# Performance work log

Hardware: AMD Instinct MI355X
Metric: run time of the kernel (lower is better)

The kernel has to match this reference:

```python
import jax, jax.numpy as jnp
import numpy as np

N_NODES = 1024
CHANNELS = [1, 64, 128]
DENSE = [196608, 256]
SAMPLE_NUMBER = 50


def _glorot(key, shape):
    fan_in, fan_out = shape[0], shape[-1]
    s = jnp.sqrt(6.0 / (fan_in + fan_out))
    return jax.random.uniform(key, shape, jnp.float32, -s, s)


def setup_inputs() -> dict:
    key = jax.random.key(0)
    ks = jax.random.split(key, 20)
    T, B = 16, 64
    inp = {
        "xs_seq": jax.random.normal(ks[0], (T, B, N_NODES, CHANNELS[0]), jnp.float32),
        "adj": jax.random.uniform(ks[1], (N_NODES, N_NODES), jnp.float32) / N_NODES,
    }
    # GCGRU params per layer: gates z, r, candidate n over concat([x, h])
    ki = 2
    for li in range(len(CHANNELS) - 1):
        cin, cout = CHANNELS[li], CHANNELS[li + 1]
        for g in ("z", "r", "n"):
            inp[f"W{g}{li}"] = _glorot(ks[ki], (cin + cout, cout)); ki += 1
            inp[f"b{g}{li}"] = jnp.zeros((cout,), jnp.float32)
    inp["W_mu"] = _glorot(ks[ki], (DENSE[0], DENSE[1])); ki += 1
    inp["b_mu"] = jnp.zeros((DENSE[1],), jnp.float32)
    inp["W_lv"] = _glorot(ks[ki], (DENSE[0], DENSE[1])); ki += 1
    inp["b_lv"] = jnp.zeros((DENSE[1],), jnp.float32)
    return inp


def _gcgru(xs, adj, Wz, bz, Wr, br, Wn, bn, cout):
    # xs: [T, B, N, cin]; graph-conv GRU over time via scan
    T, B, N, _ = xs.shape
    h0 = jnp.zeros((B, N, cout), xs.dtype)

    def gconv(a, x, W, b):  # adj @ x @ W + b
        return jnp.einsum("ij,bjc,cd->bid", a, x, W) + b

    def step(h, x):
        xh = jnp.concatenate([x, h], axis=-1)
        z = jax.nn.sigmoid(gconv(adj, xh, Wz, bz))
        r = jax.nn.sigmoid(gconv(adj, xh, Wr, br))
        xrh = jnp.concatenate([x, r * h], axis=-1)
        n = jnp.tanh(gconv(adj, xrh, Wn, bn))
        h_new = (1.0 - z) * h + z * n
        return h_new, h_new

    _, hs = jax.lax.scan(step, h0, xs)
    return hs  # [T, B, N, cout]


def _forward(xs_seq, adj, Wz0, bz0, Wr0, br0, Wn0, bn0,
             Wz1, bz1, Wr1, br1, Wn1, bn1, W_mu, b_mu, W_lv, b_lv, eps):
    h1 = _gcgru(xs_seq, adj, Wz0, bz0, Wr0, br0, Wn0, bn0, CHANNELS[1])
    h2 = _gcgru(h1, adj, Wz1, bz1, Wr1, br1, Wn1, bn1, CHANNELS[2])
    xs = jnp.concatenate([h1[-1], h2[-1]], axis=2)  # [B, N, C1+C2]
    B = xs.shape[0]
    xs = xs.reshape(B, -1)  # [B, N*(C1+C2)]
    mu = jax.nn.sigmoid(xs @ W_mu + b_mu)
    logvar = jax.nn.sigmoid(xs @ W_lv + b_lv)
    std = jnp.exp(0.5 * logvar)
    z = mu + eps * std
    return z, mu, logvar


def reference(xs_seq, adj, Wz0, bz0, Wr0, br0, Wn0, bn0,
              Wz1, bz1, Wr1, br1, Wn1, bn1, W_mu, b_mu, W_lv, b_lv):
    B = xs_seq.shape[1]
    ekey = jax.random.fold_in(jax.random.key(0), 1234)
    eps = jax.random.normal(ekey, (SAMPLE_NUMBER, B, DENSE[1]), jnp.float32).mean(0)
    return _forward(xs_seq, adj, Wz0, bz0, Wr0, br0, Wn0, bn0,
                    Wz1, bz1, Wr1, br1, Wn1, bn1, W_mu, b_mu, W_lv, b_lv, eps)
```

## Files before the change

kernel.cpp:

```cpp
#include <hip/hip_runtime.h>
#include <math.h>

#define EPS_MODE 0

typedef unsigned short u16;
typedef short bf16x8 __attribute__((ext_vector_type(8)));
typedef float f32x4 __attribute__((ext_vector_type(4)));
typedef u16 u16x4 __attribute__((ext_vector_type(4)));
typedef u16 u16x8 __attribute__((ext_vector_type(8)));

static constexpr int T = 16;
static constexpr size_t MF = 1u << 20;
static constexpr int DKCH = 512;
static constexpr int DKCHUNK = 196608 / DKCH;

__device__ __forceinline__ u16 f2bf(float f) {
  unsigned u = __float_as_uint(f);
  unsigned r = (u + 0x7fffu + ((u >> 16) & 1u)) >> 16;
  return (u16)r;
}
__device__ __forceinline__ float bf2f(u16 h) {
  return __uint_as_float(((unsigned)h) << 16);
}
__device__ __forceinline__ void gload16(const void* g, void* l) {
  __builtin_amdgcn_global_load_lds(
      (const __attribute__((address_space(1))) void*)g,
      (__attribute__((address_space(3))) void*)l, 16, 0, 0);
}
__device__ __forceinline__ float sigm(float x) { return 1.f / (1.f + expf(-x)); }

__global__ __launch_bounds__(256) void cast_bf16(const float* __restrict__ in,
                                                 u16* __restrict__ out, int n) {
  int i = (blockIdx.x * 256 + threadIdx.x) * 4;
  if (i < n) {
    float4 v = *reinterpret_cast<const float4*>(&in[i]);
    out[i + 0] = f2bf(v.x); out[i + 1] = f2bf(v.y);
    out[i + 2] = f2bf(v.z); out[i + 3] = f2bf(v.w);
  }
}

__global__ __launch_bounds__(256) void prep_wt(const float* __restrict__ Wz0, const float* __restrict__ Wr0,
                                               const float* __restrict__ Wn0, const float* __restrict__ Wz1,
                                               const float* __restrict__ Wr1, const float* __restrict__ Wn1,
                                               u16* __restrict__ WzrT0, u16* __restrict__ WnT0,
                                               u16* __restrict__ WzrT1, u16* __restrict__ WnT1) {
  int seg = blockIdx.y;
  int idx = blockIdx.x * 256 + threadIdx.x;
  if (seg == 0) {
    if (idx < 128 * 64) {
      int j = idx >> 6, k = idx & 63;
      float v = (j < 64) ? Wz0[(k + 1) * 64 + j] : Wr0[(k + 1) * 64 + (j - 64)];
      WzrT0[idx] = f2bf(v);
    }
  } else if (seg == 1) {
    if (idx < 64 * 64) {
      int j = idx >> 6, k = idx & 63;
      WnT0[idx] = f2bf(Wn0[(k + 1) * 64 + j]);
    }
  } else if (seg == 2) {
    if (idx < 256 * 192) {
      int j = idx / 192, k = idx % 192;
      float v = (j < 128) ? Wz1[k * 128 + j] : Wr1[k * 128 + (j - 128)];
      WzrT1[idx] = f2bf(v);
    }
  } else {
    if (idx < 128 * 192) {
      int j = idx / 192, k = idx % 192;
      WnT1[idx] = f2bf(Wn1[k * 128 + j]);
    }
  }
}

__global__ __launch_bounds__(256) void init0(const float* __restrict__ AXv,
                                             const float* __restrict__ Wz0,
                                             const float* __restrict__ bz0,
                                             const float* __restrict__ Wn0,
                                             const float* __restrict__ bn0,
                                             u16* __restrict__ h1T) {
  int b = blockIdx.x, n0 = blockIdx.y * 256;
  __shared__ float axs[256];
  int tid = threadIdx.x;
  if (tid < 64)
    *(float4*)&axs[tid * 4] = *(const float4*)&AXv[((size_t)b << 10) + n0 + tid * 4];
  __syncthreads();
  int cb = tid >> 6, nl = (tid & 63) * 4;
  for (int c0 = 0; c0 < 64; c0 += 4) {
    int c = c0 + cb;
    float wz = Wz0[c], bz = bz0[c], wn = Wn0[c], bn = bn0[c];
    u16x4 pk;
#pragma unroll
    for (int j = 0; j < 4; ++j) {
      float ax = axs[nl + j];
      float z = sigm(fmaf(ax, wz, bz));
      pk[j] = f2bf(z * tanhf(fmaf(ax, wn, bn)));
    }
    *(u16x4*)&h1T[((((size_t)b << 6) + c) << 10) + n0 + nl] = pk;
  }
}

template <int EPI, int LOGC, int MFR>
__device__ __forceinline__ void dev_adj_mfma(int bx, int by, char* lds,
                                             const u16* __restrict__ A,
                                             const u16* __restrict__ BT,
                                             void* __restrict__ OUT) {
  constexpr int MT = MFR * 32;
  int tid = threadIdx.x;
  int w = tid >> 6, lane = tid & 63;
  int row0 = by * MT, col0 = bx * 128;
  int wm = w >> 1, wn = w & 1;
  f32x4 acc[MFR][4] = {};
  for (int k0 = 0; k0 < 1024; k0 += 64) {
#pragma unroll
    for (int q = 0; q < MFR; ++q) {
      int row = q * 32 + w * 8 + (lane >> 3);
      gload16(A + (size_t)(row0 + row) * 1024 + k0 + (lane & 7) * 8,
              lds + q * 4096 + w * 1024);
    }
#pragma unroll
    for (int q = 0; q < 4; ++q) {
      int row = q * 32 + w * 8 + (lane >> 3);
      gload16(BT + (size_t)(col0 + row) * 1024 + k0 + (lane & 7) * 8,
              lds + MFR * 4096 + q * 4096 + w * 1024);
    }
    __syncthreads();
#pragma unroll
    for (int kk = 0; kk < 2; ++kk) {
      bf16x8 a[MFR], bb[4];
#pragma unroll
      for (int m = 0; m < MFR; ++m)
        a[m] = *(const bf16x8*)(lds + (wm * (MFR * 16) + m * 16 + (lane & 15)) * 128 + kk * 64 + (lane >> 4) * 16);
#pragma unroll
      for (int n = 0; n < 4; ++n)
        bb[n] = *(const bf16x8*)(lds + MFR * 4096 + (wn * 64 + n * 16 + (lane & 15)) * 128 + kk * 64 + (lane >> 4) * 16);
#pragma unroll
      for (int m = 0; m < MFR; ++m)
#pragma unroll
        for (int n = 0; n < 4; ++n)
          acc[m][n] = __builtin_amdgcn_mfma_f32_16x16x32_bf16(a[m], bb[n], acc[m][n], 0, 0, 0);
    }
    __syncthreads();
  }
  if (EPI == 1) {
    float* O = (float*)OUT;
#pragma unroll
    for (int m = 0; m < MFR; ++m)
#pragma unroll
      for (int n = 0; n < 4; ++n) {
        int col = col0 + wn * 64 + n * 16 + (lane & 15);
        int t = col >> 6, bbx = col & 63;
        int row = row0 + wm * (MFR * 16) + m * 16 + ((lane >> 4) << 2);
        *(float4*)&O[((size_t)t << 16) + ((size_t)bbx << 10) + row] = *(float4*)&acc[m][n];
      }
  } else {
    u16* O = (u16*)OUT;
    constexpr int C = 1 << LOGC;
#pragma unroll
    for (int m = 0; m < MFR; ++m)
#pragma unroll
      for (int n = 0; n < 4; ++n) {
        int col = col0 + wn * 64 + n * 16 + (lane & 15);
        int bbx = col >> LOGC, c = col & (C - 1);
#pragma unroll
        for (int j = 0; j < 4; ++j) {
          int row = row0 + wm * (MFR * 16) + m * 16 + ((lane >> 4) << 2) + j;
          O[(((size_t)bbx << 10) + row) * C + c] = f2bf(acc[m][n][j]);
        }
      }
  }
}

template <int EPI, int LOGC, int MFR>
__global__ __launch_bounds__(256) void adj_mfma(const u16* __restrict__ A,
                                                const u16* __restrict__ BT,
                                                void* __restrict__ OUT) {
  __shared__ __align__(16) char lds[(MFR + 4) * 4096];
  dev_adj_mfma<EPI, LOGC, MFR>(blockIdx.x, blockIdx.y, lds, A, BT, OUT);
}

template <int C, int RK1, int MFR>
__device__ __forceinline__ void dev_adj_ngate(
    int bx, int by, char* lds,
    const u16* __restrict__ A, const u16* __restrict__ BT,
    const u16* __restrict__ WnT, const float* __restrict__ bias,
    const float* __restrict__ axv, const float* __restrict__ wx,
    const u16* __restrict__ AH1, const u16* __restrict__ zT,
    u16* __restrict__ hT) {
  constexpr int LOGC = (C == 64) ? 6 : 7;
  constexpr int KW = (C == 64) ? 64 : 192;
  constexpr int KKAN = C / 32;
  constexpr int MT = MFR * 32;
  int tid = threadIdx.x;
  int w = tid >> 6, lane = tid & 63;
  int row0 = by * MT, col0 = bx * 128;
  int wm = w >> 1, wn = w & 1;
  f32x4 acc[MFR][4] = {};
  for (int k0 = 0; k0 < 1024; k0 += 64) {
#pragma unroll
    for (int q = 0; q < MFR; ++q) {
      int row = q * 32 + w * 8 + (lane >> 3);
      gload16(A + (size_t)(row0 + row) * 1024 + k0 + (lane & 7) * 8,
              lds + q * 4096 + w * 1024);
    }
#pragma unroll
    for (int q = 0; q < 4; ++q) {
      int row = q * 32 + w * 8 + (lane >> 3);
      gload16(BT + (size_t)(col0 + row) * 1024 + k0 + (lane & 7) * 8,
              lds + MFR * 4096 + q * 4096 + w * 1024);
    }
    __syncthreads();
#pragma unroll
    for (int kk = 0; kk < 2; ++kk) {
      bf16x8 a[MFR], bb[4];
#pragma unroll
      for (int m = 0; m < MFR; ++m)
        a[m] = *(const bf16x8*)(lds + (wm * (MFR * 16) + m * 16 + (lane & 15)) * 128 + kk * 64 + (lane >> 4) * 16);
#pragma unroll
      for (int n = 0; n < 4; ++n)
        bb[n] = *(const bf16x8*)(lds + MFR * 4096 + (wn * 64 + n * 16 + (lane & 15)) * 128 + kk * 64 + (lane >> 4) * 16);
#pragma unroll
      for (int m = 0; m < MFR; ++m)
#pragma unroll
        for (int n = 0; n < 4; ++n)
          acc[m][n] = __builtin_amdgcn_mfma_f32_16x16x32_bf16(a[m], bb[n], acc[m][n], 0, 0, 0);
    }
    __syncthreads();
  }
  u16* ANt = (u16*)lds;
#pragma unroll
  for (int m = 0; m < MFR; ++m)
#pragma unroll
    for (int n = 0; n < 4; ++n) {
      int cl = wn * 64 + n * 16 + (lane & 15);
      int rl = wm * (MFR * 16) + m * 16 + ((lane >> 4) << 2);
#pragma unroll
      for (int j = 0; j < 4; ++j)
        ANt[(rl + j) * 136 + cl] = f2bf(acc[m][n][j]);
    }
  __syncthreads();
  int wrow = w >> 1, half = w & 1;
  int arow0 = wrow * (MFR * 16);
  int b0 = col0 >> LOGC;
  int out0 = (C == 64) ? 0 : half * 64;
  int kbase = (C == 64) ? half * 64 : 0;
  int b_eff = (C == 64) ? (b0 + half) : b0;
  constexpr int WOFF = (C == 64) ? 0 : 64;
  f32x4 acc2[MFR][4] = {};
#pragma unroll
  for (int kk = 0; kk < KKAN; ++kk) {
    bf16x8 a[MFR], bb[4];
    int ka = kbase + kk * 32 + (lane >> 4) * 8;
#pragma unroll
    for (int m = 0; m < MFR; ++m)
      a[m] = *(const bf16x8*)&ANt[(arow0 + m * 16 + (lane & 15)) * 136 + ka];
#pragma unroll
    for (int n = 0; n < 4; ++n)
      bb[n] = *(const bf16x8*)&WnT[(size_t)(out0 + n * 16 + (lane & 15)) * KW + WOFF + kk * 32 + (lane >> 4) * 8];
#pragma unroll
    for (int m = 0; m < MFR; ++m)
#pragma unroll
      for (int n = 0; n < 4; ++n)
        acc2[m][n] = __builtin_amdgcn_mfma_f32_16x16x32_bf16(a[m], bb[n], acc2[m][n], 0, 0, 0);
  }
  if (C == 128) {
#pragma unroll
    for (int kk = 0; kk < 2; ++kk) {
      bf16x8 a[MFR], bb[4];
#pragma unroll
      for (int m = 0; m < MFR; ++m)
        a[m] = *(const bf16x8*)&AH1[(((size_t)b0 << 10) + row0 + arow0 + m * 16 + (lane & 15)) * 64 + kk * 32 + (lane >> 4) * 8];
#pragma unroll
      for (int n = 0; n < 4; ++n)
        bb[n] = *(const bf16x8*)&WnT[(size_t)(out0 + n * 16 + (lane & 15)) * 192 + kk * 32 + (lane >> 4) * 8];
#pragma unroll
      for (int m = 0; m < MFR; ++m)
#pragma unroll
        for (int n = 0; n < 4; ++n)
          acc2[m][n] = __builtin_amdgcn_mfma_f32_16x16x32_bf16(a[m], bb[n], acc2[m][n], 0, 0, 0);
    }
  }
#pragma unroll
  for (int m = 0; m < MFR; ++m) {
    float ax4[4];
    if (RK1) {
      float4 v = *(const float4*)&axv[((size_t)b_eff << 10) + row0 + arow0 + m * 16 + ((lane >> 4) << 2)];
      ax4[0] = v.x; ax4[1] = v.y; ax4[2] = v.z; ax4[3] = v.w;
    }
#pragma unroll
    for (int n = 0; n < 4; ++n) {
      int cp = out0 + n * 16 + (lane & 15);
      int grow = arow0 + m * 16 + ((lane >> 4) << 2);
      size_t idx = (((size_t)b_eff << LOGC) + cp) * 1024 + row0 + grow;
      u16x4 zv = *(const u16x4*)&zT[idx];
      u16x4 hv = *(const u16x4*)&hT[idx];
      u16x4 pk;
#pragma unroll
      for (int j = 0; j < 4; ++j) {
        float g = acc2[m][n][j] + bias[cp];
        if (RK1) g += ax4[j] * wx[cp];
        float nv = tanhf(g);
        float z = bf2f(zv[j]), ho = bf2f(hv[j]);
        pk[j] = f2bf((1.f - z) * ho + z * nv);
      }
      *(u16x4*)&hT[idx] = pk;
    }
  }
}

template <int C, int RK1, int MFR>
__global__ __launch_bounds__(256) void adj_ngate(
    const u16* __restrict__ A, const u16* __restrict__ BT,
    const u16* __restrict__ WnT, const float* __restrict__ bias,
    const float* __restrict__ axv, const float* __restrict__ wx,
    const u16* __restrict__ AH1, const u16* __restrict__ zT,
    u16* __restrict__ hT) {
  constexpr int MT = MFR * 32;
  constexpr int STG = (MFR + 4) * 4096;
  constexpr int ANB = MT * 136 * 2;
  constexpr int LDSZ = STG > ANB ? STG : ANB;
  __shared__ __align__(16) char lds[LDSZ];
  dev_adj_ngate<C, RK1, MFR>(blockIdx.x, blockIdx.y, lds, A, BT, WnT, bias, axv, wx,
                             AH1, zT, hT);
}

__global__ __launch_bounds__(256) void combo_tail(
    const u16* __restrict__ adjB, const u16* __restrict__ h2T, u16* __restrict__ AH2,
    const u16* __restrict__ rh0T, const u16* __restrict__ WnT0, const float* __restrict__ bn0,
    const float* __restrict__ AXt1, const float* __restrict__ Wn0,
    const u16* __restrict__ z0T, u16* __restrict__ h1T) {
  __shared__ __align__(16) char lds[32768];
  int bid = blockIdx.x;
  if (bid < 512) {
    dev_adj_mfma<0, 7, 4>(bid & 63, bid >> 6, lds, adjB, h2T, AH2);
  } else {
    int b2 = bid - 512;
    dev_adj_ngate<64, 1, 2>(b2 & 31, b2 >> 5, lds, adjB, rh0T, WnT0, bn0,
                            AXt1, Wn0, nullptr, z0T, h1T);
  }
}

__global__ __launch_bounds__(256) void ah1_zr(
    const u16* __restrict__ adjB, const u16* __restrict__ h1T,
    const u16* __restrict__ AH2, const u16* __restrict__ h2T,
    const u16* __restrict__ WzrT1, const float* __restrict__ bz1, const float* __restrict__ br1,
    const u16* __restrict__ WzrT0, const float* __restrict__ bz0, const float* __restrict__ br0,
    const float* __restrict__ AXt1, const float* __restrict__ wz0x, const float* __restrict__ wr0x,
    u16* __restrict__ AH1, u16* __restrict__ z1T, u16* __restrict__ rh1T,
    u16* __restrict__ z0T, u16* __restrict__ rh0T, int do_zr0) {
  __shared__ __align__(16) char lds[24576];
  int tid = threadIdx.x, w = tid >> 6, lane = tid & 63;
  int row0 = blockIdx.y * 64, col0 = blockIdx.x * 128;
  int b0 = col0 >> 6;
  int wm = w >> 1, wn = w & 1;
  f32x4 acc[2][4] = {};
  for (int k0 = 0; k0 < 1024; k0 += 64) {
#pragma unroll
    for (int q = 0; q < 2; ++q) {
      int row = q * 32 + w * 8 + (lane >> 3);
      gload16(adjB + (size_t)(row0 + row) * 1024 + k0 + (lane & 7) * 8,
              lds + q * 4096 + w * 1024);
    }
#pragma unroll
    for (int q = 0; q < 4; ++q) {
      int row = q * 32 + w * 8 + (lane >> 3);
      gload16(h1T + (size_t)(col0 + row) * 1024 + k0 + (lane & 7) * 8,
              lds + 8192 + q * 4096 + w * 1024);
    }
    __syncthreads();
#pragma unroll
    for (int kk = 0; kk < 2; ++kk) {
      bf16x8 a[2], bb[4];
#pragma unroll
      for (int m = 0; m < 2; ++m)
        a[m] = *(const bf16x8*)(lds + (wm * 32 + m * 16 + (lane & 15)) * 128 + kk * 64 + (lane >> 4) * 16);
#pragma unroll
      for (int n = 0; n < 4; ++n)
        bb[n] = *(const bf16x8*)(lds + 8192 + (wn * 64 + n * 16 + (lane & 15)) * 128 + kk * 64 + (lane >> 4) * 16);
#pragma unroll
      for (int m = 0; m < 2; ++m)
#pragma unroll
        for (int n = 0; n < 4; ++n)
          acc[m][n] = __builtin_amdgcn_mfma_f32_16x16x32_bf16(a[m], bb[n], acc[m][n], 0, 0, 0);
    }
    __syncthreads();
  }
  u16* ANt = (u16*)lds;
#pragma unroll
  for (int m = 0; m < 2; ++m)
#pragma unroll
    for (int n = 0; n < 4; ++n) {
      int col = wn * 64 + n * 16 + (lane & 15);
      int bl = col >> 6, c = col & 63;
      int rl = wm * 32 + m * 16 + ((lane >> 4) << 2);
#pragma unroll
      for (int j = 0; j < 4; ++j) {
        u16 v = f2bf(acc[m][n][j]);
        AH1[(((size_t)(b0 + bl) << 10) + row0 + rl + j) * 64 + c] = v;
        ANt[(bl * 64 + rl + j) * 72 + c] = v;
      }
    }
  __syncthreads();
  int b = b0 + wm;
#pragma unroll
  for (int hz = 0; hz < 2; ++hz) {
    f32x4 g1[4][4] = {};
#pragma unroll
    for (int kk = 0; kk < 2; ++kk) {
      bf16x8 a[4], bb[4];
#pragma unroll
      for (int m = 0; m < 4; ++m)
        a[m] = *(const bf16x8*)&ANt[(wm * 64 + m * 16 + (lane & 15)) * 72 + kk * 32 + (lane >> 4) * 8];
#pragma unroll
      for (int n = 0; n < 4; ++n) {
        int out = hz * 128 + wn * 64 + n * 16 + (lane & 15);
        bb[n] = *(const bf16x8*)&WzrT1[(size_t)out * 192 + kk * 32 + (lane >> 4) * 8];
      }
#pragma unroll
      for (int m = 0; m < 4; ++m)
#pragma unroll
        for (int n = 0; n < 4; ++n)
          g1[m][n] = __builtin_amdgcn_mfma_f32_16x16x32_bf16(a[m], bb[n], g1[m][n], 0, 0, 0);
    }
#pragma unroll
    for (int kk = 0; kk < 4; ++kk) {
      bf16x8 a[4], bb[4];
#pragma unroll
      for (int m = 0; m < 4; ++m) {
        int gn = row0 + m * 16 + (lane & 15);
        a[m] = *(const bf16x8*)&AH2[(((size_t)b << 10) + gn) * 128 + kk * 32 + (lane >> 4) * 8];
      }
#pragma unroll
      for (int n = 0; n < 4; ++n) {
        int out = hz * 128 + wn * 64 + n * 16 + (lane & 15);
        bb[n] = *(const bf16x8*)&WzrT1[(size_t)out * 192 + 64 + kk * 32 + (lane >> 4) * 8];
      }
#pragma unroll
      for (int m = 0; m < 4; ++m)
#pragma unroll
        for (int n = 0; n < 4; ++n)
          g1[m][n] = __builtin_amdgcn_mfma_f32_16x16x32_bf16(a[m], bb[n], g1[m][n], 0, 0, 0);
    }
#pragma unroll
    for (int m = 0; m < 4; ++m)
#pragma unroll
      for (int n = 0; n < 4; ++n) {
        int outq = hz * 128 + wn * 64 + n * 16 + (lane & 15);
        bool iz = outq < 128;
        int c = iz ? outq : outq - 128;
        int gr = m * 16 + ((lane >> 4) << 2);
        size_t idx = (((size_t)b * 128 + c) << 10) + row0 + gr;
        u16x4 hv;
        if (!iz) hv = *(const u16x4*)&h2T[idx];
        u16x4 pk;
#pragma unroll
        for (int j = 0; j < 4; ++j) {
          float g = g1[m][n][j] + (iz ? bz1 : br1)[c];
          float sg = sigm(g);
          pk[j] = iz ? f2bf(sg) : f2bf(sg * bf2f(hv[j]));
        }
        *(u16x4*)&(iz ? z1T : rh1T)[idx] = pk;
      }
  }
  if (do_zr0) {
    f32x4 g0[4][4] = {};
#pragma unroll
    for (int kk = 0; kk < 2; ++kk) {
      bf16x8 a[4], bb[4];
#pragma unroll
      for (int m = 0; m < 4; ++m)
        a[m] = *(const bf16x8*)&ANt[(wm * 64 + m * 16 + (lane & 15)) * 72 + kk * 32 + (lane >> 4) * 8];
#pragma unroll
      for (int n = 0; n < 4; ++n) {
        int out = wn * 64 + n * 16 + (lane & 15);
        bb[n] = *(const bf16x8*)&WzrT0[(size_t)out * 64 + kk * 32 + (lane >> 4) * 8];
      }
#pragma unroll
      for (int m = 0; m < 4; ++m)
#pragma unroll
        for (int n = 0; n < 4; ++n)
          g0[m][n] = __builtin_amdgcn_mfma_f32_16x16x32_bf16(a[m], bb[n], g0[m][n], 0, 0, 0);
    }
#pragma unroll
    for (int m = 0; m < 4; ++m) {
      int gr0 = m * 16 + ((lane >> 4) << 2);
      float4 av = *(const float4*)&AXt1[((size_t)b << 10) + row0 + gr0];
      float ax4[4] = {av.x, av.y, av.z, av.w};
#pragma unroll
      for (int n = 0; n < 4; ++n) {
        int out = wn * 64 + n * 16 + (lane & 15);
        bool iz = out < 64;
        int c = out & 63;
        size_t idx = (((size_t)b * 64 + c) << 10) + row0 + gr0;
        u16x4 hv;
        if (!iz) hv = *(const u16x4*)&h1T[idx];
        u16x4 pk;
#pragma unroll
        for (int j = 0; j < 4; ++j) {
          float g = g0[m][n][j] + (iz ? bz0 : br0)[c] + ax4[j] * (iz ? wz0x : wr0x)[c];
          float sg = sigm(g);
          pk[j] = iz ? f2bf(sg) : f2bf(sg * bf2f(hv[j]));
        }
        *(u16x4*)&(iz ? z0T : rh0T)[idx] = pk;
      }
    }
  }
}

__global__ __launch_bounds__(256) void transpose_x(const u16* __restrict__ h1T,
                                                   const u16* __restrict__ h2T,
                                                   u16* __restrict__ X) {
  int b = blockIdx.x;
  int n0 = blockIdx.y * 128;
  __shared__ u16 tile[192][136];
  int tid = threadIdx.x;
#pragma unroll
  for (int i = 0; i < 12; ++i) {
    int id = tid + i * 256;
    int c = id >> 4, g = id & 15;
    u16x8 v;
    if (c < 64) v = *(const u16x8*)&h1T[(((size_t)b << 6) + c) * 1024 + n0 + g * 8];
    else        v = *(const u16x8*)&h2T[(((size_t)b << 7) + (c - 64)) * 1024 + n0 + g * 8];
    *(u16x8*)&tile[c][g * 8] = v;
  }
  __syncthreads();
#pragma unroll
  for (int i = 0; i < 12; ++i) {
    int id = tid + i * 256;
    int n = id / 24, g = id % 24;
    u16x8 v;
#pragma unroll
    for (int j = 0; j < 8; ++j) v[j] = tile[g * 8 + j][n];
    *(u16x8*)&X[(size_t)b * 196608 + (size_t)(n0 + n) * 192 + g * 8] = v;
  }
}

__global__ __launch_bounds__(256) void dense_mfma4(const u16* __restrict__ X,
                                                   const float* __restrict__ Wmu,
                                                   const float* __restrict__ Wlv,
                                                   float* __restrict__ P) {
  __shared__ __align__(16) char lds[8192 + 128 * 70 * 2];
  u16* Bs = (u16*)(lds + 8192);
  int tid = threadIdx.x, w = tid >> 6, lane = tid & 63;
  int o0 = blockIdx.x * 128;
  int ch = blockIdx.y, mat = blockIdx.z;
  const float* W = mat ? Wlv : Wmu;
  int kb = ch * DKCHUNK;
  int oq = (tid & 31) * 4;
  int kq = (tid >> 5) * 8;
  f32x4 acc[4][2] = {};
  float4 wv[8];
  {
    const float* wp = W + (size_t)(kb + kq) * 256 + o0 + oq;
#pragma unroll
    for (int p = 0; p < 8; ++p) wv[p] = *(const float4*)(wp + (size_t)p * 256);
  }
  for (int s = 0; s < DKCHUNK / 64; ++s) {
    int kg = kb + s * 64;
#pragma unroll
    for (int q = 0; q < 2; ++q) {
      int row = q * 32 + w * 8 + (lane >> 3);
      gload16(X + (size_t)row * 196608 + kg + (lane & 7) * 8,
              lds + q * 4096 + w * 1024);
    }
#pragma unroll
    for (int j = 0; j < 4; ++j) {
      u16x8 pk;
#pragma unroll
      for (int p = 0; p < 8; ++p) pk[p] = f2bf(wv[p][j]);
      *(u16x8*)&Bs[(oq + j) * 70 + kq] = pk;
    }
    __syncthreads();
    if (s + 1 < DKCHUNK / 64) {
      const float* wp = W + (size_t)(kg + 64 + kq) * 256 + o0 + oq;
#pragma unroll
      for (int p = 0; p < 8; ++p) wv[p] = *(const float4*)(wp + (size_t)p * 256);
    }
#pragma unroll
    for (int kk = 0; kk < 2; ++kk) {
      bf16x8 a[4], bb[2];
#pragma unroll
      for (int m = 0; m < 4; ++m)
        a[m] = *(const bf16x8*)(lds + (m * 16 + (lane & 15)) * 128 + kk * 64 + (lane >> 4) * 16);
#pragma unroll
      for (int n = 0; n < 2; ++n) {
        int o = w * 32 + n * 16 + (lane & 15);
        bb[n] = *(const bf16x8*)&Bs[o * 70 + kk * 32 + (lane >> 4) * 8];
      }
#pragma unroll
      for (int m = 0; m < 4; ++m)
#pragma unroll
        for (int n = 0; n < 2; ++n)
          acc[m][n] = __builtin_amdgcn_mfma_f32_16x16x32_bf16(a[m], bb[n], acc[m][n], 0, 0, 0);
    }
    __syncthreads();
  }
#pragma unroll
  for (int m = 0; m < 4; ++m)
#pragma unroll
    for (int n = 0; n < 2; ++n) {
      int o = o0 + w * 32 + n * 16 + (lane & 15);
#pragma unroll
      for (int j = 0; j < 4; ++j) {
        int row = m * 16 + ((lane >> 4) << 2) + j;
        P[(((size_t)mat * DKCH + ch) * 64 + row) * 256 + o] = acc[m][n][j];
      }
    }
}

__device__ __forceinline__ unsigned rotl32(unsigned v, int s) {
  return (v << s) | (v >> (32 - s));
}
__device__ void threefry(unsigned k0, unsigned k1, unsigned x0, unsigned x1,
                         unsigned& o0, unsigned& o1) {
  unsigned ks2 = k0 ^ k1 ^ 0x1BD11BDAu;
  unsigned a = x0 + k0, b = x1 + k1;
#define TF_RND(rot) { a += b; b = rotl32(b, rot); b ^= a; }
  TF_RND(13) TF_RND(15) TF_RND(26) TF_RND(6)
  a += k1; b += ks2 + 1u;
  TF_RND(17) TF_RND(29) TF_RND(16) TF_RND(24)
  a += ks2; b += k0 + 2u;
  TF_RND(13) TF_RND(15) TF_RND(26) TF_RND(6)
  a += k0; b += k1 + 3u;
  TF_RND(17) TF_RND(29) TF_RND(16) TF_RND(24)
  a += k1; b += ks2 + 4u;
  TF_RND(13) TF_RND(15) TF_RND(26) TF_RND(6)
  a += ks2; b += k0 + 5u;
#undef TF_RND
  o0 = a; o1 = b;
}

__device__ float u32_to_normal(unsigned bits) {
  unsigned fb = (bits >> 9) | 0x3F800000u;
  float f = __uint_as_float(fb) - 1.0f;
  const float lo = -0.99999994f;
  float u = f * 2.0f + lo;
  u = fmaxf(lo, u);
  float w = -log1pf(-u * u);
  float p;
  if (w < 5.0f) {
    w -= 2.5f;
    p = 2.81022636e-08f;
    p = fmaf(p, w, 3.43273939e-07f);
    p = fmaf(p, w, -3.5233877e-06f);
    p = fmaf(p, w, -4.39150654e-06f);
    p = fmaf(p, w, 0.00021858087f);
    p = fmaf(p, w, -0.00125372503f);
    p = fmaf(p, w, -0.00417768164f);
    p = fmaf(p, w, 0.246640727f);
    p = fmaf(p, w, 1.50140941f);
  } else {
    w = sqrtf(w) - 3.0f;
    p = -0.000200214257f;
    p = fmaf(p, w, 0.000100950558f);
    p = fmaf(p, w, 0.00134934322f);
    p = fmaf(p, w, -0.00367342844f);
    p = fmaf(p, w, 0.00573950773f);
    p = fmaf(p, w, -0.0076224613f);
    p = fmaf(p, w, 0.00943887047f);
    p = fmaf(p, w, 1.00167406f);
    p = fmaf(p, w, 2.83297682f);
  }
  return 1.41421354f * (p * u);
}

__global__ __launch_bounds__(256) void eps_kernel(float* __restrict__ eps) {
  int b = blockIdx.x;
  int o = threadIdx.x;
  unsigned k0, k1;
  threefry(0u, 0u, 0u, 1234u, k0, k1);
  float s = 0.f;
  for (int smp = 0; smp < 50; ++smp) {
    unsigned idx = ((unsigned)smp * 64u + (unsigned)b) * 256u + (unsigned)o;
    unsigned o0, o1, bits;
#if EPS_MODE == 0
    threefry(k0, k1, 0u, idx, o0, o1);
    bits = o0 ^ o1;
#else
    unsigned pp = idx % 409600u, half = idx / 409600u;
    threefry(k0, k1, pp, pp + 409600u, o0, o1);
    bits = half ? o1 : o0;
#endif
    s += u32_to_normal(bits);
  }
  eps[b * 256 + o] = s / 50.0f;
}

__global__ __launch_bounds__(256) void final_kernel(const float* __restrict__ P,
                                                    const float* __restrict__ bmu,
                                                    const float* __restrict__ blv,
                                                    const float* __restrict__ eps,
                                                    float* __restrict__ out) {
  int b = blockIdx.x, o = threadIdx.x;
  float smu = 0.f, slv = 0.f;
  for (int ch = 0; ch < DKCH; ++ch) {
    smu += P[(((size_t)0 * DKCH + ch) * 64 + b) * 256 + o];
    slv += P[(((size_t)1 * DKCH + ch) * 64 + b) * 256 + o];
  }
  float mu = sigm(smu + bmu[o]);
  float lv = sigm(slv + blv[o]);
  float z = mu + eps[b * 256 + o] * expf(0.5f * lv);
  out[b * 256 + o] = z;
  out[16384 + b * 256 + o] = mu;
  out[32768 + b * 256 + o] = lv;
}

extern "C" void kernel_launch(void* const* d_in, const int* in_sizes, int n_in,
                              void* d_out, int out_size, void* d_ws, size_t ws_size,
                              hipStream_t stream) {
  (void)in_sizes; (void)n_in; (void)out_size; (void)ws_size;
  const float* xs  = (const float*)d_in[0];
  const float* adj = (const float*)d_in[1];
  const float* Wz0 = (const float*)d_in[2];  const float* bz0 = (const float*)d_in[3];
  const float* Wr0 = (const float*)d_in[4];  const float* br0 = (const float*)d_in[5];
  const float* Wn0 = (const float*)d_in[6];  const float* bn0 = (const float*)d_in[7];
  const float* Wz1 = (const float*)d_in[8];  const float* bz1 = (const float*)d_in[9];
  const float* Wr1 = (const float*)d_in[10]; const float* br1 = (const float*)d_in[11];
  const float* Wn1 = (const float*)d_in[12]; const float* bn1 = (const float*)d_in[13];
  const float* Wmu = (const float*)d_in[14]; const float* bmu = (const float*)d_in[15];
  const float* Wlv = (const float*)d_in[16]; const float* blv = (const float*)d_in[17];

  float* ws = (float*)d_ws;
  u16*  adjB  = (u16*)(ws);
  u16*  xsB   = (u16*)(ws + MF / 2);
  float* AXv  = ws + 1 * MF;
  u16*  h1T   = (u16*)(ws + 2 * MF);
  u16*  h2T   = (u16*)(ws + 4 * MF);
  u16*  z0T   = (u16*)(ws + 8 * MF);
  u16*  z1T   = (u16*)(ws + 10 * MF);
  u16*  rh0T  = (u16*)(ws + 14 * MF);
  u16*  rh1T  = (u16*)(ws + 16 * MF);
  u16*  AH1   = (u16*)(ws + 20 * MF);
  u16*  AH2   = (u16*)(ws + 22 * MF);
  u16*  WTb   = (u16*)(ws + 26 * MF);
  u16*  X     = (u16*)(ws + 8 * MF);
  float* P    = ws + 16 * MF;
  float* EPS  = ws + 33 * MF;

  u16* WzrT0 = WTb;
  u16* WnT0  = WTb + 8192;
  u16* WzrT1 = WTb + 12288;
  u16* WnT1  = WTb + 61440;

  hipMemsetAsync(ws + 4 * MF, 0, 4 * MF * sizeof(float), stream);
  hipMemsetAsync(ws + 22 * MF, 0, 4 * MF * sizeof(float), stream);

  cast_bf16<<<1024, 256, 0, stream>>>(adj, adjB, 1 << 20);
  cast_bf16<<<1024, 256, 0, stream>>>(xs, xsB, 1 << 20);
  prep_wt<<<dim3(192, 4), 256, 0, stream>>>(Wz0, Wr0, Wn0, Wz1, Wr1, Wn1,
                                            WzrT0, WnT0, WzrT1, WnT1);

  adj_mfma<1, 0, 4><<<dim3(8, 8), 256, 0, stream>>>(adjB, xsB, AXv);

  init0<<<dim3(64, 4), 256, 0, stream>>>(AXv, Wz0, bz0, Wn0, bn0, h1T);

  for (int t = 0; t < T; ++t) {
    const float* AXn = AXv + (size_t)((t + 1 < T) ? t + 1 : t) * 65536;
    ah1_zr<<<dim3(32, 16), 256, 0, stream>>>(
        adjB, h1T, AH2, h2T, WzrT1, bz1, br1, WzrT0, bz0, br0,
        AXn, Wz0, Wr0, AH1, z1T, rh1T, z0T, rh0T, (t + 1 < T) ? 1 : 0);
    adj_ngate<128, 0, 4><<<dim3(64, 8), 256, 0, stream>>>(
        adjB, rh1T, WnT1, bn1, nullptr, nullptr, AH1, z1T, h2T);
    if (t + 1 < T)
      combo_tail<<<1024, 256, 0, stream>>>(adjB, h2T, AH2, rh0T, WnT0, bn0,
                                           AXn, Wn0, z0T, h1T);
  }

  transpose_x<<<dim3(64, 8), 256, 0, stream>>>(h1T, h2T, X);
  dense_mfma4<<<dim3(2, DKCH, 2), 256, 0, stream>>>(X, Wmu, Wlv, P);
  eps_kernel<<<64, 256, 0, stream>>>(EPS);
  final_kernel<<<64, 256, 0, stream>>>(P, bmu, blv, EPS, (float*)d_out);
}
```

Before: 2.716 ms.

## Fuse per-timestep kernel launches into one cooperative persistent kernel

Replaces the 47 per-timestep launches of three kernels with a single cooperative kernel of 1024 blocks. Inside it, grid-wide syncs separate the three phases of each GRU step. The aim is to remove kernel launch and drain overhead across the recurrence. In exchange all blocks must be co-resident (launch bounds 256,4 may limit registers), and every block pays the grid.sync cost even in phases where it is idle.

```diff
diff --git a/kernel.cpp b/kernel.cpp
--- a/kernel.cpp
+++ b/kernel.cpp
@@ -1,7 +1,10 @@
 #include <hip/hip_runtime.h>
+#include <hip/hip_cooperative_groups.h>
 #include <math.h>
 
 #define EPS_MODE 0
+
+namespace cg = cooperative_groups;
 
 typedef unsigned short u16;
 typedef short bf16x8 __attribute__((ext_vector_type(8)));
@@ -306,39 +309,8 @@
   }
 }
 
-template <int C, int RK1, int MFR>
-__global__ __launch_bounds__(256) void adj_ngate(
-    const u16* __restrict__ A, const u16* __restrict__ BT,
-    const u16* __restrict__ WnT, const float* __restrict__ bias,
-    const float* __restrict__ axv, const float* __restrict__ wx,
-    const u16* __restrict__ AH1, const u16* __restrict__ zT,
-    u16* __restrict__ hT) {
-  constexpr int MT = MFR * 32;
-  constexpr int STG = (MFR + 4) * 4096;
-  constexpr int ANB = MT * 136 * 2;
-  constexpr int LDSZ = STG > ANB ? STG : ANB;
-  __shared__ __align__(16) char lds[LDSZ];
-  dev_adj_ngate<C, RK1, MFR>(blockIdx.x, blockIdx.y, lds, A, BT, WnT, bias, axv, wx,
-                             AH1, zT, hT);
-}
-
-__global__ __launch_bounds__(256) void combo_tail(
-    const u16* __restrict__ adjB, const u16* __restrict__ h2T, u16* __restrict__ AH2,
-    const u16* __restrict__ rh0T, const u16* __restrict__ WnT0, const float* __restrict__ bn0,
-    const float* __restrict__ AXt1, const float* __restrict__ Wn0,
-    const u16* __restrict__ z0T, u16* __restrict__ h1T) {
-  __shared__ __align__(16) char lds[32768];
-  int bid = blockIdx.x;
-  if (bid < 512) {
-    dev_adj_mfma<0, 7, 4>(bid & 63, bid >> 6, lds, adjB, h2T, AH2);
-  } else {
-    int b2 = bid - 512;
-    dev_adj_ngate<64, 1, 2>(b2 & 31, b2 >> 5, lds, adjB, rh0T, WnT0, bn0,
-                            AXt1, Wn0, nullptr, z0T, h1T);
-  }
-}
-
-__global__ __launch_bounds__(256) void ah1_zr(
+__device__ __forceinline__ void dev_ah1_zr(
+    int bx, int by, char* lds,
     const u16* __restrict__ adjB, const u16* __restrict__ h1T,
     const u16* __restrict__ AH2, const u16* __restrict__ h2T,
     const u16* __restrict__ WzrT1, const float* __restrict__ bz1, const float* __restrict__ br1,
@@ -346,9 +318,8 @@
     const float* __restrict__ AXt1, const float* __restrict__ wz0x, const float* __restrict__ wr0x,
     u16* __restrict__ AH1, u16* __restrict__ z1T, u16* __restrict__ rh1T,
     u16* __restrict__ z0T, u16* __restrict__ rh0T, int do_zr0) {
-  __shared__ __align__(16) char lds[24576];
   int tid = threadIdx.x, w = tid >> 6, lane = tid & 63;
-  int row0 = blockIdx.y * 64, col0 = blockIdx.x * 128;
+  int row0 = by * 64, col0 = bx * 128;
   int b0 = col0 >> 6;
   int wm = w >> 1, wn = w & 1;
   f32x4 acc[2][4] = {};
@@ -501,6 +472,39 @@
         }
         *(u16x4*)&(iz ? z0T : rh0T)[idx] = pk;
       }
+    }
+  }
+}
+
+__global__ __launch_bounds__(256, 4) void loop_coop(
+    const u16* adjB, u16* h1T, u16* h2T,
+    const u16* WzrT0, const u16* WnT0, const u16* WzrT1, const u16* WnT1,
+    const float* bz0, const float* br0, const float* bn0,
+    const float* bz1, const float* br1, const float* bn1,
+    const float* Wz0, const float* Wr0, const float* Wn0,
+    const float* AXv,
+    u16* AH1, u16* AH2, u16* z0T, u16* z1T, u16* rh0T, u16* rh1T) {
+  __shared__ __align__(16) char lds[34816];
+  cg::grid_group grid = cg::this_grid();
+  int bid = blockIdx.x;
+  for (int t = 0; t < T; ++t) {
+    const float* AXn = AXv + (size_t)((t + 1 < T) ? t + 1 : t) * 65536;
+    int do0 = (t + 1 < T) ? 1 : 0;
+    if (bid < 512)
+      dev_ah1_zr(bid & 31, bid >> 5, lds, adjB, h1T, AH2, h2T, WzrT1, bz1, br1,
+                 WzrT0, bz0, br0, AXn, Wz0, Wr0, AH1, z1T, rh1T, z0T, rh0T, do0);
+    grid.sync();
+    if (bid < 512)
+      dev_adj_ngate<128, 0, 4>(bid & 63, bid >> 6, lds, adjB, rh1T, WnT1, bn1,
+                               nullptr, nullptr, AH1, z1T, h2T);
+    grid.sync();
+    if (t + 1 < T) {
+      if (bid < 512)
+        dev_adj_mfma<0, 7, 4>(bid & 63, bid >> 6, lds, adjB, h2T, AH2);
+      else
+        dev_adj_ngate<64, 1, 2>((bid - 512) & 31, (bid - 512) >> 5, lds, adjB,
+                                rh0T, WnT0, bn0, AXn, Wn0, nullptr, z0T, h1T);
+      grid.sync();
     }
   }
 }
@@ -752,16 +756,18 @@
 
   init0<<<dim3(64, 4), 256, 0, stream>>>(AXv, Wz0, bz0, Wn0, bn0, h1T);
 
-  for (int t = 0; t < T; ++t) {
-    const float* AXn = AXv + (size_t)((t + 1 < T) ? t + 1 : t) * 65536;
-    ah1_zr<<<dim3(32, 16), 256, 0, stream>>>(
-        adjB, h1T, AH2, h2T, WzrT1, bz1, br1, WzrT0, bz0, br0,
-        AXn, Wz0, Wr0, AH1, z1T, rh1T, z0T, rh0T, (t + 1 < T) ? 1 : 0);
-    adj_ngate<128, 0, 4><<<dim3(64, 8), 256, 0, stream>>>(
-        adjB, rh1T, WnT1, bn1, nullptr, nullptr, AH1, z1T, h2T);
-    if (t + 1 < T)
-      combo_tail<<<1024, 256, 0, stream>>>(adjB, h2T, AH2, rh0T, WnT0, bn0,
-                                           AXn, Wn0, z0T, h1T);
+  {
+    void* cargs[] = {
+        (void*)&adjB, (void*)&h1T, (void*)&h2T,
+        (void*)&WzrT0, (void*)&WnT0, (void*)&WzrT1, (void*)&WnT1,
+        (void*)&bz0, (void*)&br0, (void*)&bn0,
+        (void*)&bz1, (void*)&br1, (void*)&bn1,
+        (void*)&Wz0, (void*)&Wr0, (void*)&Wn0,
+        (void*)&AXv,
+        (void*)&AH1, (void*)&AH2, (void*)&z0T, (void*)&z1T,
+        (void*)&rh0T, (void*)&rh1T};
+    hipLaunchCooperativeKernel((void*)loop_coop, dim3(1024), dim3(256), cargs, 0,
+                               stream);
   }
 
   transpose_x<<<dim3(64, 8), 256, 0, stream>>>(h1T, h2T, X);
```

Result: slower. 10.27 ms (+278.2%).
